# Performance work log

Hardware: AMD Instinct MI355X
Metric: run time of the kernel (lower is better)

## Reference

```python
import jax, jax.numpy as jnp
import numpy as np

N_NODES = 50000
IN_CH = 128
HID = 128
OUT_CH = 40
N_LAYERS = 3
N_EDGES = 600000


def setup_inputs() -> dict:
    key = jax.random.key(0)
    ks = jax.random.split(key, 4 + 5 * N_LAYERS)
    x = jax.random.normal(ks[0], (N_NODES, IN_CH), dtype=jnp.float32)
    edge_attr = jax.random.normal(ks[1], (N_EDGES, 4), dtype=jnp.float32)
    edge_index = jax.random.randint(ks[2], (2, N_EDGES), 0, N_NODES, dtype=jnp.int64)
    # Per-layer MLP params ([in->hid->hid]); in==hid so stack as [L, d, d].
    def glorot(k, fan_in, fan_out):
        s = jnp.sqrt(2.0 / (fan_in + fan_out)).astype(jnp.float32)
        return jax.random.normal(k, (fan_in, fan_out), dtype=jnp.float32) * s
    W1 = jnp.stack([glorot(ks[3 + i], IN_CH if i == 0 else HID, HID) for i in range(N_LAYERS)])
    b1 = jnp.zeros((N_LAYERS, HID), dtype=jnp.float32)
    W2 = jnp.stack([glorot(ks[3 + N_LAYERS + i], HID, HID) for i in range(N_LAYERS)])
    b2 = jnp.zeros((N_LAYERS, HID), dtype=jnp.float32)
    Wc = glorot(ks[3 + 2 * N_LAYERS], HID, OUT_CH)
    bc = jnp.zeros((OUT_CH,), dtype=jnp.float32)
    return {"x": x, "edge_attr": edge_attr, "edge_index": edge_index,
            "W1": W1, "b1": b1, "W2": W2, "b2": b2, "Wc": Wc, "bc": bc}


def reference(x, edge_attr, edge_index, W1, b1, W2, b2, Wc, bc):
    # GIN node classifier, eval mode (dropout = identity, BN = identity).
    src, dst = edge_index[0], edge_index[1]
    h = x
    for i in range(N_LAYERS):
        # GINConv (eps=0): aggregate sum of neighbor features via scatter-add.
        msgs = h[src]                                   # [E, d] gather
        aggr = jax.ops.segment_sum(msgs, dst, num_segments=N_NODES)  # [N, d]
        z = h + aggr                                    # (1+eps)*x + sum
        z = jax.nn.relu(z @ W1[i] + b1[i])              # MLP hidden
        z = z @ W2[i] + b2[i]                           # MLP out
        h = jax.nn.relu(z)                              # F.relu(conv(...))
    return h @ Wc + bc                                  # [N, OUT_CH]
```

## Files before the change

### kernel.cpp

```cpp
#include <hip/hip_runtime.h>

#define N_NODES 50000
#define IN_CH 128
#define HID 128
#define OUT_CH 40
#define N_LAYERS 3
#define N_EDGES 600000
#define DSTRIDE 64

typedef __attribute__((ext_vector_type(8))) short short8;
typedef __attribute__((ext_vector_type(4))) float floatx4;

static __device__ __forceinline__ unsigned short f32_to_bf16(float f) {
  unsigned u = __float_as_uint(f);
  unsigned r = 0x7FFFu + ((u >> 16) & 1u);
  return (unsigned short)((u + r) >> 16);
}
static __device__ __forceinline__ float bf16_to_f32(unsigned short h) {
  return __uint_as_float(((unsigned)h) << 16);
}

#define CONV_BLOCKS 6250
#define W_BLOCKS 408
#define DEG_BLOCKS 49
#define COL_MAX (N_NODES * DSTRIDE)
#define COLF_BLOCKS 3125

__global__ __launch_bounds__(256) void prep_all_kernel(
    const float* __restrict__ x, const float* __restrict__ W1,
    const float* __restrict__ W2, const float* __restrict__ Wc,
    unsigned short* __restrict__ xb, unsigned short* __restrict__ WT,
    unsigned short* __restrict__ WcT, unsigned short* __restrict__ hb1,
    int* __restrict__ deg, int* __restrict__ col) {
  const int b = blockIdx.x;
  const int t = threadIdx.x;
  if (b < CONV_BLOCKS) {
    int i = (b * 256 + t) * 4;
    if (i < N_NODES * 128) {
      float4 v = *(const float4*)(x + i);
      ushort4 o;
      o.x = f32_to_bf16(v.x); o.y = f32_to_bf16(v.y);
      o.z = f32_to_bf16(v.z); o.w = f32_to_bf16(v.w);
      *(ushort4*)(xb + i) = o;
    }
  } else if (b < CONV_BLOCKS + W_BLOCKS) {
    int o = (b - CONV_BLOCKS) * 256 + t;
    if (o < 6 * 16384) {
      int mat = o >> 14;
      int r = o & 16383;
      int n = r >> 7;
      int k = r & 127;
      const float* W = (mat < 3) ? (W1 + (size_t)mat * 16384)
                                 : (W2 + (size_t)(mat - 3) * 16384);
      WT[(size_t)mat * 16384 + (size_t)n * 128 + k] =
          f32_to_bf16(W[(size_t)k * 128 + n]);
    } else if (o < 6 * 16384 + 48 * 128) {
      int r = o - 6 * 16384;
      int n = r >> 7;
      int k = r & 127;
      float v = (n < OUT_CH) ? Wc[(size_t)k * OUT_CH + n] : 0.0f;
      WcT[(size_t)n * 128 + k] = f32_to_bf16(v);
    }
  } else if (b < CONV_BLOCKS + W_BLOCKS + DEG_BLOCKS) {
    int i = ((b - CONV_BLOCKS - W_BLOCKS) * 256 + t) * 4;
    if (i + 3 < N_NODES) {
      *(int4*)(deg + i) = make_int4(0, 0, 0, 0);
    } else {
      for (int k = 0; k < 4; ++k)
        if (i + k < N_NODES) deg[i + k] = 0;
    }
  } else if (b < CONV_BLOCKS + W_BLOCKS + DEG_BLOCKS + COLF_BLOCKS) {
    int i = ((b - CONV_BLOCKS - W_BLOCKS - DEG_BLOCKS) * 256 + t) * 4;
    *(int4*)(col + i) = make_int4(N_NODES, N_NODES, N_NODES, N_NODES);
  } else {
    if (t < 128) xb[(size_t)N_NODES * 128 + t] = 0;
    else hb1[(size_t)N_NODES * 128 + (t - 128)] = 0;
  }
}

__global__ __launch_bounds__(256) void csr_kernel(
    const int* __restrict__ ei, int* __restrict__ deg, int* __restrict__ col) {
  int e = blockIdx.x * 256 + threadIdx.x;
  if (e >= N_EDGES) return;
  int s = ei[e];
  int d = ei[N_EDGES + e];
  int pos = atomicAdd(&deg[d], 1);
  col[(size_t)d * DSTRIDE + pos] = s;
}

__global__ __launch_bounds__(256) void aggregate_kernel(
    const unsigned short* __restrict__ h, const int* __restrict__ deg,
    const int* __restrict__ col, unsigned short* __restrict__ z) {
  int n = __builtin_amdgcn_readfirstlane(blockIdx.x * 4 + (threadIdx.x >> 6));
  int q = threadIdx.x & 63;
  const size_t co = (size_t)q * 2;
  ushort2 sv = *(const ushort2*)(h + (size_t)n * 128 + co);
  float ax[8], ay[8];
#pragma unroll
  for (int k = 0; k < 8; ++k) { ax[k] = 0.f; ay[k] = 0.f; }
  ax[0] = bf16_to_f32(sv.x);
  ay[0] = bf16_to_f32(sv.y);
  int dg = __builtin_amdgcn_readfirstlane(deg[n]);
  int cnt = (dg + 15) & ~15;
  const int* cp = col + (size_t)n * DSTRIDE;
  for (int i = 0; i < cnt; i += 16) {
    int ss[16];
#pragma unroll
    for (int k = 0; k < 16; ++k)
      ss[k] = __builtin_amdgcn_readfirstlane(cp[i + k]);
    ushort2 vv[16];
#pragma unroll
    for (int k = 0; k < 16; ++k)
      vv[k] = *(const ushort2*)(h + (size_t)ss[k] * 128 + co);
#pragma unroll
    for (int k = 0; k < 16; ++k) {
      ax[k & 7] += bf16_to_f32(vv[k].x);
      ay[k & 7] += bf16_to_f32(vv[k].y);
    }
  }
  float s0 = (ax[0] + ax[1]) + (ax[2] + ax[3]) + (ax[4] + ax[5]) + (ax[6] + ax[7]);
  float s1 = (ay[0] + ay[1]) + (ay[2] + ay[3]) + (ay[4] + ay[5]) + (ay[6] + ay[7]);
  ushort2 o;
  o.x = f32_to_bf16(s0);
  o.y = f32_to_bf16(s1);
  *(ushort2*)(z + (size_t)n * 128 + co) = o;
}

template <bool LAST>
__global__ __launch_bounds__(256) void layer_pair_kernel(
    const unsigned short* __restrict__ A, const unsigned short* __restrict__ WT1,
    const float* __restrict__ b1, const unsigned short* __restrict__ WT2,
    const float* __restrict__ b2, unsigned short* __restrict__ Z,
    const unsigned short* __restrict__ WcT, const float* __restrict__ bc,
    float* __restrict__ out, int M) {
  __shared__ __align__(16) unsigned short T[128][136];
  const int tid = threadIdx.x;
  const int w = tid >> 6;
  const int lane = tid & 63;
  const int qg = lane >> 4;
  const int ln = lane & 15;
  const int row0 = blockIdx.x * 128;
  const int rbase = w * 32;

  floatx4 acc[2][8];
#pragma unroll
  for (int mt = 0; mt < 2; ++mt)
#pragma unroll
    for (int ct = 0; ct < 8; ++ct) acc[mt][ct] = (floatx4){0.f, 0.f, 0.f, 0.f};

  const int r0 = row0 + rbase + ln;
  const int r1 = r0 + 16;
  const short8 zero8 = {0, 0, 0, 0, 0, 0, 0, 0};

#pragma unroll
  for (int ks = 0; ks < 4; ++ks) {
    const int koff = ks * 32 + qg * 8;
    short8 a0 = (r0 < M) ? *(const short8*)(A + (size_t)r0 * 128 + koff) : zero8;
    short8 a1 = (r1 < M) ? *(const short8*)(A + (size_t)r1 * 128 + koff) : zero8;
#pragma unroll
    for (int ct = 0; ct < 8; ++ct) {
      short8 b = *(const short8*)(WT1 + (size_t)(ct * 16 + ln) * 128 + koff);
      acc[0][ct] = __builtin_amdgcn_mfma_f32_16x16x32_bf16(a0, b, acc[0][ct], 0, 0, 0);
      acc[1][ct] = __builtin_amdgcn_mfma_f32_16x16x32_bf16(a1, b, acc[1][ct], 0, 0, 0);
    }
  }

#pragma unroll
  for (int ct = 0; ct < 8; ++ct) {
    float bv = b1[ct * 16 + ln];
#pragma unroll
    for (int mt = 0; mt < 2; ++mt)
#pragma unroll
      for (int r = 0; r < 4; ++r) {
        float v = fmaxf(acc[mt][ct][r] + bv, 0.0f);
        T[rbase + mt * 16 + qg * 4 + r][ct * 16 + ln] = f32_to_bf16(v);
      }
  }

  floatx4 acc2[2][8];
#pragma unroll
  for (int mt = 0; mt < 2; ++mt)
#pragma unroll
    for (int ct = 0; ct < 8; ++ct) acc2[mt][ct] = (floatx4){0.f, 0.f, 0.f, 0.f};
#pragma unroll
  for (int ks = 0; ks < 4; ++ks) {
    const int koff = ks * 32 + qg * 8;
    short8 a0 = *(const short8*)&T[rbase + ln][koff];
    short8 a1 = *(const short8*)&T[rbase + 16 + ln][koff];
#pragma unroll
    for (int ct = 0; ct < 8; ++ct) {
      short8 b = *(const short8*)(WT2 + (size_t)(ct * 16 + ln) * 128 + koff);
      acc2[0][ct] = __builtin_amdgcn_mfma_f32_16x16x32_bf16(a0, b, acc2[0][ct], 0, 0, 0);
      acc2[1][ct] = __builtin_amdgcn_mfma_f32_16x16x32_bf16(a1, b, acc2[1][ct], 0, 0, 0);
    }
  }

#pragma unroll
  for (int ct = 0; ct < 8; ++ct) {
    float bv = b2[ct * 16 + ln];
#pragma unroll
    for (int mt = 0; mt < 2; ++mt)
#pragma unroll
      for (int r = 0; r < 4; ++r) {
        float v = fmaxf(acc2[mt][ct][r] + bv, 0.0f);
        T[rbase + mt * 16 + qg * 4 + r][ct * 16 + ln] = f32_to_bf16(v);
      }
  }

  if (LAST) {
    floatx4 acc3[2][3];
#pragma unroll
    for (int mt = 0; mt < 2; ++mt)
#pragma unroll
      for (int ct = 0; ct < 3; ++ct) acc3[mt][ct] = (floatx4){0.f, 0.f, 0.f, 0.f};
#pragma unroll
    for (int ks = 0; ks < 4; ++ks) {
      const int koff = ks * 32 + qg * 8;
      short8 a0 = *(const short8*)&T[rbase + ln][koff];
      short8 a1 = *(const short8*)&T[rbase + 16 + ln][koff];
#pragma unroll
      for (int ct = 0; ct < 3; ++ct) {
        short8 b = *(const short8*)(WcT + (size_t)(ct * 16 + ln) * 128 + koff);
        acc3[0][ct] = __builtin_amdgcn_mfma_f32_16x16x32_bf16(a0, b, acc3[0][ct], 0, 0, 0);
        acc3[1][ct] = __builtin_amdgcn_mfma_f32_16x16x32_bf16(a1, b, acc3[1][ct], 0, 0, 0);
      }
    }
#pragma unroll
    for (int ct = 0; ct < 3; ++ct) {
      int colg = ct * 16 + ln;
      if (colg < OUT_CH) {
        float bv = bc[colg];
#pragma unroll
        for (int mt = 0; mt < 2; ++mt)
#pragma unroll
          for (int r = 0; r < 4; ++r) {
            int row = row0 + rbase + mt * 16 + qg * 4 + r;
            if (row < M) out[(size_t)row * OUT_CH + colg] = acc3[mt][ct][r] + bv;
          }
      }
    }
  } else {
    __syncthreads();
#pragma unroll
    for (int j = 0; j < 8; ++j) {
      int slot = tid + j * 256;
      int row = slot >> 4;
      int kb = slot & 15;
      if (row0 + row < M) {
        short8 v = *(const short8*)&T[row][kb * 8];
        *(short8*)(Z + (size_t)(row0 + row) * 128 + kb * 8) = v;
      }
    }
  }
}

extern "C" void kernel_launch(void* const* d_in, const int* in_sizes, int n_in,
                              void* d_out, int out_size, void* d_ws,
                              size_t ws_size, hipStream_t stream) {
  const float* x = (const float*)d_in[0];
  const int* ei = (const int*)d_in[2];
  const float* W1 = (const float*)d_in[3];
  const float* b1 = (const float*)d_in[4];
  const float* W2 = (const float*)d_in[5];
  const float* b2 = (const float*)d_in[6];
  const float* Wc = (const float*)d_in[7];
  const float* bc = (const float*)d_in[8];
  float* out = (float*)d_out;

  const size_t NF = (size_t)(N_NODES + 1) * 128;
  unsigned short* hb0 = (unsigned short*)d_ws;
  unsigned short* hb1 = hb0 + NF;
  unsigned short* xbf = hb1 + NF;
  unsigned short* WT = xbf + NF;
  unsigned short* WcT = WT + 6 * 16384;
  int* deg = (int*)(WcT + 48 * 128);
  int* col = deg + N_NODES;

  const dim3 blk(256);
  const int edge_grid = (N_EDGES + 255) / 256;
  const int aggr_grid = N_NODES / 4;
  const int pair_grid = (N_NODES + 127) / 128;

  prep_all_kernel<<<CONV_BLOCKS + W_BLOCKS + DEG_BLOCKS + COLF_BLOCKS + 1, blk,
                    0, stream>>>(x, W1, W2, Wc, xbf, WT, WcT, hb1, deg, col);

  csr_kernel<<<edge_grid, blk, 0, stream>>>(ei, deg, col);

  const unsigned short* h = xbf;
  for (int l = 0; l < N_LAYERS; ++l) {
    aggregate_kernel<<<aggr_grid, blk, 0, stream>>>(h, deg, col, hb0);
    if (l < N_LAYERS - 1) {
      layer_pair_kernel<false><<<pair_grid, blk, 0, stream>>>(
          hb0, WT + (size_t)l * 16384, b1 + (size_t)l * 128,
          WT + (size_t)(3 + l) * 16384, b2 + (size_t)l * 128, hb1,
          nullptr, nullptr, nullptr, N_NODES);
      h = hb1;
    } else {
      layer_pair_kernel<true><<<pair_grid, blk, 0, stream>>>(
          hb0, WT + (size_t)l * 16384, b1 + (size_t)l * 128,
          WT + (size_t)(3 + l) * 16384, b2 + (size_t)l * 128, nullptr,
          WcT, bc, out, N_NODES);
    }
  }
}
```

Before: 270.6 us.

## Stage MLP weights in LDS and halve rows per block in layer_pair_kernel

```diff
diff --git a/kernel.cpp b/kernel.cpp
--- a/kernel.cpp
+++ b/kernel.cpp
@@ -133,96 +133,95 @@
     const float* __restrict__ b2, unsigned short* __restrict__ Z,
     const unsigned short* __restrict__ WcT, const float* __restrict__ bc,
     float* __restrict__ out, int M) {
-  __shared__ __align__(16) unsigned short T[128][136];
+  __shared__ __align__(16) unsigned short Wl[128][136];
+  __shared__ __align__(16) unsigned short T[64][136];
   const int tid = threadIdx.x;
   const int w = tid >> 6;
   const int lane = tid & 63;
   const int qg = lane >> 4;
   const int ln = lane & 15;
-  const int row0 = blockIdx.x * 128;
-  const int rbase = w * 32;
-
-  floatx4 acc[2][8];
-#pragma unroll
-  for (int mt = 0; mt < 2; ++mt)
-#pragma unroll
-    for (int ct = 0; ct < 8; ++ct) acc[mt][ct] = (floatx4){0.f, 0.f, 0.f, 0.f};
-
+  const int row0 = blockIdx.x * 64;
+  const int rbase = w * 16;
   const int r0 = row0 + rbase + ln;
-  const int r1 = r0 + 16;
   const short8 zero8 = {0, 0, 0, 0, 0, 0, 0, 0};
 
+#pragma unroll
+  for (int j = 0; j < 8; ++j) {
+    int slot = tid + j * 256;
+    int row = slot >> 4;
+    int kb = slot & 15;
+    *(short8*)&Wl[row][kb * 8] = *(const short8*)(WT1 + (size_t)row * 128 + kb * 8);
+  }
+  __syncthreads();
+
+  floatx4 acc[8];
+#pragma unroll
+  for (int ct = 0; ct < 8; ++ct) acc[ct] = (floatx4){0.f, 0.f, 0.f, 0.f};
 #pragma unroll
   for (int ks = 0; ks < 4; ++ks) {
     const int koff = ks * 32 + qg * 8;
-    short8 a0 = (r0 < M) ? *(const short8*)(A + (size_t)r0 * 128 + koff) : zero8;
-    short8 a1 = (r1 < M) ? *(const short8*)(A + (size_t)r1 * 128 + koff) : zero8;
+    short8 a = (r0 < M) ? *(const short8*)(A + (size_t)r0 * 128 + koff) : zero8;
 #pragma unroll
     for (int ct = 0; ct < 8; ++ct) {
-      short8 b = *(const short8*)(WT1 + (size_t)(ct * 16 + ln) * 128 + koff);
-      acc[0][ct] = __builtin_amdgcn_mfma_f32_16x16x32_bf16(a0, b, acc[0][ct], 0, 0, 0);
-      acc[1][ct] = __builtin_amdgcn_mfma_f32_16x16x32_bf16(a1, b, acc[1][ct], 0, 0, 0);
-    }
-  }
-
+      short8 b = *(const short8*)&Wl[ct * 16 + ln][koff];
+      acc[ct] = __builtin_amdgcn_mfma_f32_16x16x32_bf16(a, b, acc[ct], 0, 0, 0);
+    }
+  }
 #pragma unroll
   for (int ct = 0; ct < 8; ++ct) {
     float bv = b1[ct * 16 + ln];
 #pragma unroll
-    for (int mt = 0; mt < 2; ++mt)
-#pragma unroll
-      for (int r = 0; r < 4; ++r) {
-        float v = fmaxf(acc[mt][ct][r] + bv, 0.0f);
-        T[rbase + mt * 16 + qg * 4 + r][ct * 16 + ln] = f32_to_bf16(v);
-      }
-  }
-
-  floatx4 acc2[2][8];
-#pragma unroll
-  for (int mt = 0; mt < 2; ++mt)
-#pragma unroll
-    for (int ct = 0; ct < 8; ++ct) acc2[mt][ct] = (floatx4){0.f, 0.f, 0.f, 0.f};
+    for (int r = 0; r < 4; ++r) {
+      float v = fmaxf(acc[ct][r] + bv, 0.0f);
+      T[rbase + qg * 4 + r][ct * 16 + ln] = f32_to_bf16(v);
+    }
+  }
+
+  __syncthreads();
+#pragma unroll
+  for (int j = 0; j < 8; ++j) {
+    int slot = tid + j * 256;
+    int row = slot >> 4;
+    int kb = slot & 15;
+    *(short8*)&Wl[row][kb * 8] = *(const short8*)(WT2 + (size_t)row * 128 + kb * 8);
+  }
+  __syncthreads();
+
+  floatx4 acc2[8];
+#pragma unroll
+  for (int ct = 0; ct < 8; ++ct) acc2[ct] = (floatx4){0.f, 0.f, 0.f, 0.f};
 #pragma unroll
   for (int ks = 0; ks < 4; ++ks) {
     const int koff = ks * 32 + qg * 8;
-    short8 a0 = *(const short8*)&T[rbase + ln][koff];
-    short8 a1 = *(const short8*)&T[rbase + 16 + ln][koff];
+    short8 a = *(const short8*)&T[rbase + ln][koff];
 #pragma unroll
     for (int ct = 0; ct < 8; ++ct) {
-      short8 b = *(const short8*)(WT2 + (size_t)(ct * 16 + ln) * 128 + koff);
-      acc2[0][ct] = __builtin_amdgcn_mfma_f32_16x16x32_bf16(a0, b, acc2[0][ct], 0, 0, 0);
-      acc2[1][ct] = __builtin_amdgcn_mfma_f32_16x16x32_bf16(a1, b, acc2[1][ct], 0, 0, 0);
-    }
-  }
-
+      short8 b = *(const short8*)&Wl[ct * 16 + ln][koff];
+      acc2[ct] = __builtin_amdgcn_mfma_f32_16x16x32_bf16(a, b, acc2[ct], 0, 0, 0);
+    }
+  }
 #pragma unroll
   for (int ct = 0; ct < 8; ++ct) {
     float bv = b2[ct * 16 + ln];
 #pragma unroll
-    for (int mt = 0; mt < 2; ++mt)
-#pragma unroll
-      for (int r = 0; r < 4; ++r) {
-        float v = fmaxf(acc2[mt][ct][r] + bv, 0.0f);
-        T[rbase + mt * 16 + qg * 4 + r][ct * 16 + ln] = f32_to_bf16(v);
-      }
+    for (int r = 0; r < 4; ++r) {
+      float v = fmaxf(acc2[ct][r] + bv, 0.0f);
+      T[rbase + qg * 4 + r][ct * 16 + ln] = f32_to_bf16(v);
+    }
   }
 
   if (LAST) {
-    floatx4 acc3[2][3];
-#pragma unroll
-    for (int mt = 0; mt < 2; ++mt)
-#pragma unroll
-      for (int ct = 0; ct < 3; ++ct) acc3[mt][ct] = (floatx4){0.f, 0.f, 0.f, 0.f};
+    floatx4 acc3[3];
+#pragma unroll
+    for (int ct = 0; ct < 3; ++ct) acc3[ct] = (floatx4){0.f, 0.f, 0.f, 0.f};
 #pragma unroll
     for (int ks = 0; ks < 4; ++ks) {
       const int koff = ks * 32 + qg * 8;
-      short8 a0 = *(const short8*)&T[rbase + ln][koff];
-      short8 a1 = *(const short8*)&T[rbase + 16 + ln][koff];
+      short8 a = *(const short8*)&T[rbase + ln][koff];
 #pragma unroll
       for (int ct = 0; ct < 3; ++ct) {
         short8 b = *(const short8*)(WcT + (size_t)(ct * 16 + ln) * 128 + koff);
-        acc3[0][ct] = __builtin_amdgcn_mfma_f32_16x16x32_bf16(a0, b, acc3[0][ct], 0, 0, 0);
-        acc3[1][ct] = __builtin_amdgcn_mfma_f32_16x16x32_bf16(a1, b, acc3[1][ct], 0, 0, 0);
+        acc3[ct] = __builtin_amdgcn_mfma_f32_16x16x32_bf16(a, b, acc3[ct], 0, 0, 0);
       }
     }
 #pragma unroll
@@ -231,18 +230,16 @@
       if (colg < OUT_CH) {
         float bv = bc[colg];
 #pragma unroll
-        for (int mt = 0; mt < 2; ++mt)
-#pragma unroll
-          for (int r = 0; r < 4; ++r) {
-            int row = row0 + rbase + mt * 16 + qg * 4 + r;
-            if (row < M) out[(size_t)row * OUT_CH + colg] = acc3[mt][ct][r] + bv;
-          }
+        for (int r = 0; r < 4; ++r) {
+          int row = row0 + rbase + qg * 4 + r;
+          if (row < M) out[(size_t)row * OUT_CH + colg] = acc3[ct][r] + bv;
+        }
       }
     }
   } else {
     __syncthreads();
 #pragma unroll
-    for (int j = 0; j < 8; ++j) {
+    for (int j = 0; j < 4; ++j) {
       int slot = tid + j * 256;
       int row = slot >> 4;
       int kb = slot & 15;
@@ -279,7 +276,7 @@
   const dim3 blk(256);
   const int edge_grid = (N_EDGES + 255) / 256;
   const int aggr_grid = N_NODES / 4;
-  const int pair_grid = (N_NODES + 127) / 128;
+  const int pair_grid = (N_NODES + 63) / 64;
 
   prep_all_kernel<<<CONV_BLOCKS + W_BLOCKS + DEG_BLOCKS + COLF_BLOCKS + 1, blk,
                     0, stream>>>(x, W1, W2, Wc, xbf, WT, WcT, hb1, deg, col);
```

New measurement: 251.2 us. 7.2% less time.
